# Kernel tuning notes

Hardware: AMD Instinct MI355X
Metric: run time of the kernel (lower is better)

Reference implementation:

```python
import jax, jax.numpy as jnp
import numpy as np

# Fixed average-trace buffer from the module (length 120)
AVG = jnp.asarray([0.0256,0.0823,0.1157,0.1315,0.1366,0.1369,0.1347,0.1308,0.1259,0.1205,0.1146,0.1086,0.1028,0.097,0.0913,0.0858,0.0805,0.0756,0.0708,0.0664,0.0623,0.0584,0.0549,0.0515,0.0485,0.0456,0.0429,0.0404,0.0381,0.036,0.034,0.0321,0.0304,0.0287,0.0272,0.0258,0.0245,0.0233,0.0222,0.0211,0.0201,0.0191,0.0182,0.0173,0.0165,0.0158,0.015,0.0143,0.0137,0.013,0.0125,0.0119,0.0114,0.0108,0.0104,0.0099,0.0095,0.0091,0.0087,0.0083,0.008,0.0077,0.0074,0.0071,0.0068,0.0065,0.0062,0.006,0.0058,0.0055,0.0053,0.005,0.0049,0.0047,0.0045,0.0044,0.0042,0.004,0.0039,0.0038,0.0036,0.0034,0.0033,0.0032,0.0031,0.003,0.0029,0.0028,0.0027,0.0026,0.0025,0.0024,0.0023,0.0022,0.0021,0.0021,0.002,0.0019,0.0018,0.0018,0.0017,0.0017,0.0016,0.0016,0.0015,0.0015,0.0014,0.0014,0.0013,0.0013,0.0013,0.0012,0.0012,0.0011,0.0011,0.0011,0.001,0.001,0.001,0.0009], dtype=jnp.float32)


def _lstm(x, w_ih, w_hh, b):
    """PyTorch-semantics single-layer LSTM. x: [N,T,D], w_ih: [4H,D], w_hh: [4H,H], b: [4H] (= b_ih + b_hh). Gate order i,f,g,o."""
    xp = jnp.einsum('ntd,gd->ntg', x, w_ih) + b  # precompute input projections: [N,T,4H]
    N = x.shape[0]
    H = w_hh.shape[1]
    h0 = jnp.zeros((N, H), x.dtype)

    def step(carry, xt):
        h, c = carry
        g = xt + h @ w_hh.T  # [N,4H]
        i, f, gg, o = jnp.split(g, 4, axis=-1)
        c = jax.nn.sigmoid(f) * c + jax.nn.sigmoid(i) * jnp.tanh(gg)
        h = jax.nn.sigmoid(o) * jnp.tanh(c)
        return (h, c), h

    _, hs = jax.lax.scan(step, (h0, h0), jnp.swapaxes(xp, 0, 1))  # hs: [T,N,H]
    return jnp.swapaxes(hs, 0, 1)  # [N,T,H]


def setup_inputs() -> dict:
    key = jax.random.key(0)
    ks = jax.random.split(key, 7)
    N, F, H = 32768, 12, 30
    s1 = 1.0 / float(np.sqrt(H))  # torch LSTM init: U(-1/sqrt(H), 1/sqrt(H))
    s2 = 1.0                      # second LSTM hidden=1 -> scale 1
    return {
        'features': jax.random.normal(ks[0], (N, F), jnp.float32),
        'w_ih1': jax.random.uniform(ks[1], (4 * H, F + 1), jnp.float32, -s1, s1),
        'w_hh1': jax.random.uniform(ks[2], (4 * H, H), jnp.float32, -s1, s1),
        'b1': jax.random.uniform(ks[3], (4 * H,), jnp.float32, -s1, s1),
        'w_ih2': jax.random.uniform(ks[4], (4, H), jnp.float32, -s2, s2),
        'w_hh2': jax.random.uniform(ks[5], (4, 1), jnp.float32, -s2, s2),
        'b2': jax.random.uniform(ks[6], (4,), jnp.float32, -s2, s2),
    }


def reference(features, w_ih1, w_hh1, b1, w_ih2, w_hh2, b2):
    N, F = features.shape
    T = AVG.shape[0]  # 120
    x = jnp.broadcast_to(features[:, None, :], (N, T, F))          # repeat features over time
    trace = jnp.broadcast_to(AVG[None, :, None], (N, T, 1))        # average trace channel
    x = jnp.concatenate([x, trace], axis=2)                        # [N,120,13]
    h1 = _lstm(x, w_ih1, w_hh1, b1)                                # [N,120,30]
    return _lstm(h1, w_ih2, w_hh2, b2)                             # [N,120,1]
```

## Files before the change

kernel.cpp:

```cpp
#include <hip/hip_runtime.h>

typedef __attribute__((ext_vector_type(8))) short bf16x8;
typedef __attribute__((ext_vector_type(4))) float f32x4;

#define LOG2E 1.44269504088896340736f

__device__ __constant__ float AVG_D[120] = {
    0.0256f,0.0823f,0.1157f,0.1315f,0.1366f,0.1369f,0.1347f,0.1308f,0.1259f,0.1205f,
    0.1146f,0.1086f,0.1028f,0.0970f,0.0913f,0.0858f,0.0805f,0.0756f,0.0708f,0.0664f,
    0.0623f,0.0584f,0.0549f,0.0515f,0.0485f,0.0456f,0.0429f,0.0404f,0.0381f,0.0360f,
    0.0340f,0.0321f,0.0304f,0.0287f,0.0272f,0.0258f,0.0245f,0.0233f,0.0222f,0.0211f,
    0.0201f,0.0191f,0.0182f,0.0173f,0.0165f,0.0158f,0.0150f,0.0143f,0.0137f,0.0130f,
    0.0125f,0.0119f,0.0114f,0.0108f,0.0104f,0.0099f,0.0095f,0.0091f,0.0087f,0.0083f,
    0.0080f,0.0077f,0.0074f,0.0071f,0.0068f,0.0065f,0.0062f,0.0060f,0.0058f,0.0055f,
    0.0053f,0.0050f,0.0049f,0.0047f,0.0045f,0.0044f,0.0042f,0.0040f,0.0039f,0.0038f,
    0.0036f,0.0034f,0.0033f,0.0032f,0.0031f,0.0030f,0.0029f,0.0028f,0.0027f,0.0026f,
    0.0025f,0.0024f,0.0023f,0.0022f,0.0021f,0.0021f,0.0020f,0.0019f,0.0018f,0.0018f,
    0.0017f,0.0017f,0.0016f,0.0016f,0.0015f,0.0015f,0.0014f,0.0014f,0.0013f,0.0013f,
    0.0013f,0.0012f,0.0012f,0.0011f,0.0011f,0.0011f,0.0010f,0.0010f,0.0010f,0.0009f
};

__device__ __forceinline__ float sig2(float x) {
    return __builtin_amdgcn_rcpf(1.0f + __builtin_amdgcn_exp2f(x));
}
__device__ __forceinline__ float tanh2(float x) {
    return fmaf(2.0f, __builtin_amdgcn_rcpf(1.0f + __builtin_amdgcn_exp2f(x)), -1.0f);
}
__device__ __forceinline__ unsigned short tb(float x) {
    return (unsigned short)(__float_as_uint(x) >> 16);
}
__device__ __forceinline__ float fb(unsigned short h) {
    return __uint_as_float(((unsigned)h) << 16);
}

__global__ void pack_weights(const float* __restrict__ w_ih1,
                             const float* __restrict__ w_hh1,
                             const float* __restrict__ b1,
                             const float* __restrict__ w_ih2,
                             const float* __restrict__ b2,
                             float* __restrict__ ws) {
    unsigned short* whi = (unsigned short*)ws;
    unsigned short* wlo = (unsigned short*)(ws + 2048);
    float* bconst = ws + 4096;
    float* wih1f  = ws + 4224;
    unsigned* avgpk = (unsigned*)(ws + 5760);
    const int tid = threadIdx.x;
    for (int idx = tid; idx < 4096; idx += 256) {
        const int T = idx >> 9, lane = (idx >> 3) & 63, j = idx & 7;
        const int r = 16 * T + (lane & 15);
        const int k = ((lane >> 4) & 3) * 8 + j;
        const int u = r >> 2, q = r & 3;
        const float sc = (q == 2) ? (-2.0f * LOG2E) : (-LOG2E);
        float v = 0.0f;
        if (u < 30) {
            if (k < 30)       v = w_hh1[(q * 30 + u) * 30 + k];
            else if (k == 30) v = w_ih1[(q * 30 + u) * 13 + 12];
        } else if (u == 30 && k < 30) {
            v = w_ih2[q * 30 + k];
        }
        v *= sc;
        const unsigned short hi = tb(v);
        whi[idx] = hi;
        wlo[idx] = tb(v - fb(hi));
    }
    for (int r = tid; r < 128; r += 256) {
        const int u = r >> 2, q = r & 3;
        const float sc = (q == 2) ? (-2.0f * LOG2E) : (-LOG2E);
        bconst[r] = sc * ((u < 30) ? b1[q * 30 + u] : ((u == 30) ? b2[q] : 0.0f));
    }
    for (int idx = tid; idx < 1536; idx += 256) {
        const int r = idx / 12, d = idx % 12;
        const int u = r >> 2, q = r & 3;
        const float sc = (q == 2) ? (-2.0f * LOG2E) : (-LOG2E);
        wih1f[idx] = (u < 30) ? sc * w_ih1[(q * 30 + u) * 13 + d] : 0.0f;
    }
    for (int t = tid; t < 121; t += 256) {
        const float a = (t < 120) ? AVG_D[t] : 0.0f;
        const unsigned short hi = tb(a);
        const unsigned short lo = tb(a - fb(hi));
        avgpk[t] = (unsigned)hi | ((unsigned)lo << 16);
    }
}

__global__ __launch_bounds__(128, 4)
void lstm_mfma_kernel(const float* __restrict__ feat,
                      const float* __restrict__ w_hh2,
                      const float* __restrict__ ws,
                      float* __restrict__ out) {
    __shared__ __align__(16) unsigned hx[2][16 * 36];
    __shared__ __align__(16) float out_s[16 * 124];

    const int tid  = threadIdx.x;
    const int lane = tid & 63;
    const int wr   = __builtin_amdgcn_readfirstlane(tid >> 6);
    const int s    = lane & 15;
    const int quad = lane >> 4;
    const int seq  = blockIdx.x * 16 + s;
    const unsigned* avgpk = (const unsigned*)(ws + 5760);

    for (int i = tid; i < 1152; i += 128) (&hx[0][0])[i] = 0u;
    __syncthreads();
    if (tid < 16) hx[0][tid * 36 + 30] = avgpk[0];

    bf16x8 Ahi[4], Alo[4];
    {
        const unsigned short* whi = (const unsigned short*)ws;
        const unsigned short* wlo = (const unsigned short*)(ws + 2048);
#pragma unroll
        for (int Tl = 0; Tl < 4; Tl++) {
            Ahi[Tl] = *(const bf16x8*)(whi + (4 * wr + Tl) * 512 + lane * 8);
            Alo[Tl] = *(const bf16x8*)(wlo + (4 * wr + Tl) * 512 + lane * 8);
        }
    }

    float f0[12];
    {
        const float4* fp = reinterpret_cast<const float4*>(feat + seq * 12);
        float4 A = fp[0], B = fp[1], C = fp[2];
        f0[0]=A.x; f0[1]=A.y; f0[2]=A.z; f0[3]=A.w;
        f0[4]=B.x; f0[5]=B.y; f0[6]=B.z; f0[7]=B.w;
        f0[8]=C.x; f0[9]=C.y; f0[10]=C.z; f0[11]=C.w;
    }
    f32x4 projb[4];
    {
        const float* bconst = ws + 4096;
        const float* wih1f  = ws + 4224;
#pragma unroll
        for (int Tl = 0; Tl < 4; Tl++) {
#pragma unroll
            for (int g = 0; g < 4; g++) {
                const int r = 64 * wr + 16 * Tl + 4 * quad + g;
                float acc = bconst[r];
#pragma unroll
                for (int d = 0; d < 12; d++) acc = fmaf(f0[d], wih1f[r * 12 + d], acc);
                projb[Tl][g] = acc;
            }
        }
    }

    float c1[4];
#pragma unroll
    for (int Tl = 0; Tl < 4; Tl++) c1[Tl] = 0.0f;
    float h2 = 0.0f, c2 = 0.0f;
    const float whs0 = -LOG2E * w_hh2[0];
    const float whs1 = -LOG2E * w_hh2[1];
    const float whs2 = -2.0f * LOG2E * w_hh2[2];
    const float whs3 = -LOG2E * w_hh2[3];

    __syncthreads();

#pragma unroll 1
    for (int t = 0; t <= 120; t++) {
        const int buf = t & 1;
        const unsigned* hb = hx[buf];
        unsigned*       hn = hx[buf ^ 1];

        const uint4 Ra = *reinterpret_cast<const uint4*>(hb + s * 36 + 8 * quad);
        const uint4 Rb = *reinterpret_cast<const uint4*>(hb + s * 36 + 8 * quad + 4);
        union { int4 i; bf16x8 v; } ubh, ubl;
        ubh.i.x = (int)__builtin_amdgcn_perm(Ra.y, Ra.x, 0x05040100u);
        ubh.i.y = (int)__builtin_amdgcn_perm(Ra.w, Ra.z, 0x05040100u);
        ubh.i.z = (int)__builtin_amdgcn_perm(Rb.y, Rb.x, 0x05040100u);
        ubh.i.w = (int)__builtin_amdgcn_perm(Rb.w, Rb.z, 0x05040100u);
        ubl.i.x = (int)__builtin_amdgcn_perm(Ra.y, Ra.x, 0x07060302u);
        ubl.i.y = (int)__builtin_amdgcn_perm(Ra.w, Ra.z, 0x07060302u);
        ubl.i.z = (int)__builtin_amdgcn_perm(Rb.y, Rb.x, 0x07060302u);
        ubl.i.w = (int)__builtin_amdgcn_perm(Rb.w, Rb.z, 0x07060302u);
        const bf16x8 Bhi = ubh.v, Blo = ubl.v;

        f32x4 D[4];
#pragma unroll
        for (int Tl = 0; Tl < 4; Tl++)
            D[Tl] = __builtin_amdgcn_mfma_f32_16x16x32_bf16(Alo[Tl], Bhi, projb[Tl], 0, 0, 0);
#pragma unroll
        for (int Tl = 0; Tl < 4; Tl++)
            D[Tl] = __builtin_amdgcn_mfma_f32_16x16x32_bf16(Ahi[Tl], Blo, D[Tl], 0, 0, 0);
#pragma unroll
        for (int Tl = 0; Tl < 4; Tl++)
            D[Tl] = __builtin_amdgcn_mfma_f32_16x16x32_bf16(Ahi[Tl], Bhi, D[Tl], 0, 0, 0);

        if (t >= 1 && wr == 1 && quad == 2) {
            const float g0 = fmaf(h2, whs0, D[3][0]);
            const float g1 = fmaf(h2, whs1, D[3][1]);
            const float g2 = fmaf(h2, whs2, D[3][2]);
            const float g3 = fmaf(h2, whs3, D[3][3]);
            c2 = sig2(g1) * c2 + sig2(g0) * tanh2(g2);
            h2 = sig2(g3) * tanh2(c2 * (-2.0f * LOG2E));
            out_s[s * 124 + (t - 1)] = h2;
        }

        if (t < 120) {
#pragma unroll
            for (int Tl = 0; Tl < 4; Tl++) {
                const int u = 16 * wr + 4 * Tl + quad;
                if (u < 30) {
                    const float ei = __builtin_amdgcn_exp2f(D[Tl][0]);
                    const float ef = __builtin_amdgcn_exp2f(D[Tl][1]);
                    const float eg = __builtin_amdgcn_exp2f(D[Tl][2]);
                    const float eo = __builtin_amdgcn_exp2f(D[Tl][3]);
                    const float pi_ = 1.0f + ei, pf = 1.0f + ef;
                    const float pg  = 1.0f + eg, po = 1.0f + eo;
                    const float pig = pi_ * pg;
                    const float num = fmaf(c1[Tl], pig, (1.0f - eg) * pf);
                    const float ck  = num * __builtin_amdgcn_rcpf(pf * pig);
                    c1[Tl] = ck;
                    float carg = -2.0f * LOG2E * ck;
                    carg = fminf(fmaxf(carg, -80.0f), 80.0f);
                    const float ec = __builtin_amdgcn_exp2f(carg);
                    const float hk = (1.0f - ec) *
                                     __builtin_amdgcn_rcpf(po * (1.0f + ec));
                    const unsigned hbits = __float_as_uint(hk);
                    const float rem = hk - __uint_as_float(hbits & 0xffff0000u);
                    hn[s * 36 + u] = __builtin_amdgcn_perm(
                        __float_as_uint(rem), hbits, 0x07060302u);
                }
            }
            if (wr == 1 && lane < 16) hn[lane * 36 + 30] = avgpk[t + 1];
        }

        __syncthreads();
    }

    float* outb = out + (size_t)blockIdx.x * 16 * 120;
#pragma unroll
    for (int it = 0; it < 4; it++) {
        const int fi = it * 128 + tid;
        if (fi < 480) {
            const int sq = fi / 30, j = fi % 30;
            const float4 v = *reinterpret_cast<const float4*>(&out_s[sq * 124 + j * 4]);
            *reinterpret_cast<float4*>(&outb[sq * 120 + j * 4]) = v;
        }
    }
}

extern "C" void kernel_launch(void* const* d_in, const int* in_sizes, int n_in,
                              void* d_out, int out_size, void* d_ws, size_t ws_size,
                              hipStream_t stream) {
    (void)in_sizes; (void)n_in; (void)out_size; (void)ws_size;
    const float* feat  = (const float*)d_in[0];
    const float* w_ih1 = (const float*)d_in[1];
    const float* w_hh1 = (const float*)d_in[2];
    const float* b1    = (const float*)d_in[3];
    const float* w_ih2 = (const float*)d_in[4];
    const float* w_hh2 = (const float*)d_in[5];
    const float* b2    = (const float*)d_in[6];
    float* ws  = (float*)d_ws;
    float* out = (float*)d_out;

    hipLaunchKernelGGL(pack_weights, dim3(1), dim3(256), 0, stream,
                       w_ih1, w_hh1, b1, w_ih2, b2, ws);
    hipLaunchKernelGGL(lstm_mfma_kernel, dim3(2048), dim3(128), 0, stream,
                       feat, w_hh2, ws, out);
}
```

Measured before the change: 257.5 us.

## Give each wave its own 16 sequences to drop per-step block barriers

Each wave now computes all 128 gate rows (8 MFMA tiles) for its own 16 sequences, so there are 32 sequences per block. The hidden-state exchange lives in a per-wave LDS buffer, which lets the per-timestep __syncthreads go away; only the final barrier before output remains. The cost is double the MFMA work and register footprint per wave (8 A tiles hi/lo, 8 accumulators), and launch bounds drop to 2 blocks per CU. Correctness now depends on intra-wave LDS ordering with no barrier between timesteps.

```diff
diff --git a/kernel.cpp b/kernel.cpp
--- a/kernel.cpp
+++ b/kernel.cpp
@@ -82,34 +82,34 @@
     }
 }
 
-__global__ __launch_bounds__(128, 4)
+__global__ __launch_bounds__(128, 2)
 void lstm_mfma_kernel(const float* __restrict__ feat,
                       const float* __restrict__ w_hh2,
                       const float* __restrict__ ws,
                       float* __restrict__ out) {
-    __shared__ __align__(16) unsigned hx[2][16 * 36];
-    __shared__ __align__(16) float out_s[16 * 124];
+    __shared__ __align__(16) unsigned hx[2][2][16 * 36];
+    __shared__ __align__(16) float out_s[32 * 124];
 
     const int tid  = threadIdx.x;
     const int lane = tid & 63;
-    const int wr   = __builtin_amdgcn_readfirstlane(tid >> 6);
+    const int wv   = __builtin_amdgcn_readfirstlane(tid >> 6);
     const int s    = lane & 15;
     const int quad = lane >> 4;
-    const int seq  = blockIdx.x * 16 + s;
+    const int seq  = blockIdx.x * 32 + wv * 16 + s;
     const unsigned* avgpk = (const unsigned*)(ws + 5760);
 
-    for (int i = tid; i < 1152; i += 128) (&hx[0][0])[i] = 0u;
+    for (int i = tid; i < 2304; i += 128) (&hx[0][0][0])[i] = 0u;
     __syncthreads();
-    if (tid < 16) hx[0][tid * 36 + 30] = avgpk[0];
-
-    bf16x8 Ahi[4], Alo[4];
+    if (tid < 32) hx[tid >> 4][0][(tid & 15) * 36 + 30] = avgpk[0];
+
+    bf16x8 Ahi[8], Alo[8];
     {
         const unsigned short* whi = (const unsigned short*)ws;
         const unsigned short* wlo = (const unsigned short*)(ws + 2048);
 #pragma unroll
-        for (int Tl = 0; Tl < 4; Tl++) {
-            Ahi[Tl] = *(const bf16x8*)(whi + (4 * wr + Tl) * 512 + lane * 8);
-            Alo[Tl] = *(const bf16x8*)(wlo + (4 * wr + Tl) * 512 + lane * 8);
+        for (int T = 0; T < 8; T++) {
+            Ahi[T] = *(const bf16x8*)(whi + T * 512 + lane * 8);
+            Alo[T] = *(const bf16x8*)(wlo + T * 512 + lane * 8);
         }
     }
 
@@ -121,26 +121,26 @@
         f0[4]=B.x; f0[5]=B.y; f0[6]=B.z; f0[7]=B.w;
         f0[8]=C.x; f0[9]=C.y; f0[10]=C.z; f0[11]=C.w;
     }
-    f32x4 projb[4];
+    f32x4 projb[8];
     {
         const float* bconst = ws + 4096;
         const float* wih1f  = ws + 4224;
 #pragma unroll
-        for (int Tl = 0; Tl < 4; Tl++) {
+        for (int T = 0; T < 8; T++) {
 #pragma unroll
             for (int g = 0; g < 4; g++) {
-                const int r = 64 * wr + 16 * Tl + 4 * quad + g;
+                const int r = 16 * T + 4 * quad + g;
                 float acc = bconst[r];
 #pragma unroll
                 for (int d = 0; d < 12; d++) acc = fmaf(f0[d], wih1f[r * 12 + d], acc);
-                projb[Tl][g] = acc;
+                projb[T][g] = acc;
             }
         }
     }
 
-    float c1[4];
-#pragma unroll
-    for (int Tl = 0; Tl < 4; Tl++) c1[Tl] = 0.0f;
+    float c1[8];
+#pragma unroll
+    for (int T = 0; T < 8; T++) c1[T] = 0.0f;
     float h2 = 0.0f, c2 = 0.0f;
     const float whs0 = -LOG2E * w_hh2[0];
     const float whs1 = -LOG2E * w_hh2[1];
@@ -152,8 +152,8 @@
 #pragma unroll 1
     for (int t = 0; t <= 120; t++) {
         const int buf = t & 1;
-        const unsigned* hb = hx[buf];
-        unsigned*       hn = hx[buf ^ 1];
+        const unsigned* hb = hx[wv][buf];
+        unsigned*       hn = hx[wv][buf ^ 1];
 
         const uint4 Ra = *reinterpret_cast<const uint4*>(hb + s * 36 + 8 * quad);
         const uint4 Rb = *reinterpret_cast<const uint4*>(hb + s * 36 + 8 * quad + 4);
@@ -168,42 +168,42 @@
         ubl.i.w = (int)__builtin_amdgcn_perm(Rb.w, Rb.z, 0x07060302u);
         const bf16x8 Bhi = ubh.v, Blo = ubl.v;
 
-        f32x4 D[4];
-#pragma unroll
-        for (int Tl = 0; Tl < 4; Tl++)
-            D[Tl] = __builtin_amdgcn_mfma_f32_16x16x32_bf16(Alo[Tl], Bhi, projb[Tl], 0, 0, 0);
-#pragma unroll
-        for (int Tl = 0; Tl < 4; Tl++)
-            D[Tl] = __builtin_amdgcn_mfma_f32_16x16x32_bf16(Ahi[Tl], Blo, D[Tl], 0, 0, 0);
-#pragma unroll
-        for (int Tl = 0; Tl < 4; Tl++)
-            D[Tl] = __builtin_amdgcn_mfma_f32_16x16x32_bf16(Ahi[Tl], Bhi, D[Tl], 0, 0, 0);
-
-        if (t >= 1 && wr == 1 && quad == 2) {
-            const float g0 = fmaf(h2, whs0, D[3][0]);
-            const float g1 = fmaf(h2, whs1, D[3][1]);
-            const float g2 = fmaf(h2, whs2, D[3][2]);
-            const float g3 = fmaf(h2, whs3, D[3][3]);
+        f32x4 D[8];
+#pragma unroll
+        for (int T = 0; T < 8; T++)
+            D[T] = __builtin_amdgcn_mfma_f32_16x16x32_bf16(Alo[T], Bhi, projb[T], 0, 0, 0);
+#pragma unroll
+        for (int T = 0; T < 8; T++)
+            D[T] = __builtin_amdgcn_mfma_f32_16x16x32_bf16(Ahi[T], Blo, D[T], 0, 0, 0);
+#pragma unroll
+        for (int T = 0; T < 8; T++)
+            D[T] = __builtin_amdgcn_mfma_f32_16x16x32_bf16(Ahi[T], Bhi, D[T], 0, 0, 0);
+
+        if (t >= 1 && quad == 2) {
+            const float g0 = fmaf(h2, whs0, D[7][0]);
+            const float g1 = fmaf(h2, whs1, D[7][1]);
+            const float g2 = fmaf(h2, whs2, D[7][2]);
+            const float g3 = fmaf(h2, whs3, D[7][3]);
             c2 = sig2(g1) * c2 + sig2(g0) * tanh2(g2);
             h2 = sig2(g3) * tanh2(c2 * (-2.0f * LOG2E));
-            out_s[s * 124 + (t - 1)] = h2;
+            out_s[(wv * 16 + s) * 124 + (t - 1)] = h2;
         }
 
         if (t < 120) {
 #pragma unroll
-            for (int Tl = 0; Tl < 4; Tl++) {
-                const int u = 16 * wr + 4 * Tl + quad;
+            for (int T = 0; T < 8; T++) {
+                const int u = 4 * T + quad;
                 if (u < 30) {
-                    const float ei = __builtin_amdgcn_exp2f(D[Tl][0]);
-                    const float ef = __builtin_amdgcn_exp2f(D[Tl][1]);
-                    const float eg = __builtin_amdgcn_exp2f(D[Tl][2]);
-                    const float eo = __builtin_amdgcn_exp2f(D[Tl][3]);
+                    const float ei = __builtin_amdgcn_exp2f(D[T][0]);
+                    const float ef = __builtin_amdgcn_exp2f(D[T][1]);
+                    const float eg = __builtin_amdgcn_exp2f(D[T][2]);
+                    const float eo = __builtin_amdgcn_exp2f(D[T][3]);
                     const float pi_ = 1.0f + ei, pf = 1.0f + ef;
                     const float pg  = 1.0f + eg, po = 1.0f + eo;
                     const float pig = pi_ * pg;
-                    const float num = fmaf(c1[Tl], pig, (1.0f - eg) * pf);
+                    const float num = fmaf(c1[T], pig, (1.0f - eg) * pf);
                     const float ck  = num * __builtin_amdgcn_rcpf(pf * pig);
-                    c1[Tl] = ck;
+                    c1[T] = ck;
                     float carg = -2.0f * LOG2E * ck;
                     carg = fminf(fmaxf(carg, -80.0f), 80.0f);
                     const float ec = __builtin_amdgcn_exp2f(carg);
@@ -215,17 +215,16 @@
                         __float_as_uint(rem), hbits, 0x07060302u);
                 }
             }
-            if (wr == 1 && lane < 16) hn[lane * 36 + 30] = avgpk[t + 1];
-        }
-
-        __syncthreads();
-    }
-
-    float* outb = out + (size_t)blockIdx.x * 16 * 120;
-#pragma unroll
-    for (int it = 0; it < 4; it++) {
+            if (lane < 16) hn[lane * 36 + 30] = avgpk[t + 1];
+        }
+    }
+
+    __syncthreads();
+    float* outb = out + (size_t)blockIdx.x * 32 * 120;
+#pragma unroll
+    for (int it = 0; it < 8; it++) {
         const int fi = it * 128 + tid;
-        if (fi < 480) {
+        if (fi < 960) {
             const int sq = fi / 30, j = fi % 30;
             const float4 v = *reinterpret_cast<const float4*>(&out_s[sq * 124 + j * 4]);
             *reinterpret_cast<float4*>(&outb[sq * 120 + j * 4]) = v;
@@ -249,6 +248,6 @@
 
     hipLaunchKernelGGL(pack_weights, dim3(1), dim3(256), 0, stream,
                        w_ih1, w_hh1, b1, w_ih2, b2, ws);
-    hipLaunchKernelGGL(lstm_mfma_kernel, dim3(2048), dim3(128), 0, stream,
+    hipLaunchKernelGGL(lstm_mfma_kernel, dim3(1024), dim3(128), 0, stream,
                        feat, w_hh2, ws, out);
 }
```

Result: faster. 245.0 us (-4.9%).
